# Performance work log

Hardware: AMD Instinct MI355X
Metric: run time of the kernel (lower is better)

Reference implementation:

```python
import jax, jax.numpy as jnp
import numpy as np

BITS = 8
BOUND = 2 ** (BITS - 1) - 1  # 127, symmetric int8 as in AQT IntNumerics


def setup_inputs() -> dict:
    key = jax.random.key(0)
    k1, k2 = jax.random.split(key)
    lhs = jax.random.normal(k1, (8192, 4096), dtype=jnp.float32)
    rhs = jax.random.normal(k2, (4096, 4096), dtype=jnp.float32)
    return {"lhs": lhs, "rhs": rhs}


def reference(lhs, rhs):
    # Per-channel symmetric scales over the contracting dim (AQT calibration:
    # abs-max / bound). lhs contracts axis 1, rhs contracts axis 0, per
    # dimension_numbers (((1,),(0,)),((),())).
    lhs_scale = jnp.max(jnp.abs(lhs), axis=1, keepdims=True) / BOUND  # [M,1]
    rhs_scale = jnp.max(jnp.abs(rhs), axis=0, keepdims=True) / BOUND  # [1,N]
    lhs_scale = jnp.where(lhs_scale == 0, jnp.ones_like(lhs_scale), lhs_scale)
    rhs_scale = jnp.where(rhs_scale == 0, jnp.ones_like(rhs_scale), rhs_scale)

    # Quantize: round-to-nearest, clip to [-127, 127], store as int8.
    qlhs = jnp.clip(jnp.round(lhs / lhs_scale), -BOUND, BOUND).astype(jnp.int8)
    qrhs = jnp.clip(jnp.round(rhs / rhs_scale), -BOUND, BOUND).astype(jnp.int8)

    # Integer matmul with int32 accumulation (the AQT quantized dot_general).
    acc = jax.lax.dot_general(
        qlhs, qrhs,
        dimension_numbers=(((1,), (0,)), ((), ())),
        preferred_element_type=jnp.int32,
    )  # [M, N] int32

    # Inline dequant by transposed scales (scale_t): [M,1] * [1,N].
    return acc.astype(jnp.float32) * lhs_scale * rhs_scale
```

## Files before the change

kernel.cpp:

```cpp
#include <hip/hip_runtime.h>
#include <stdint.h>

#define M_DIM 8192
#define N_DIM 4096
#define K_DIM 4096

typedef int v4i __attribute__((ext_vector_type(4)));

typedef __attribute__((address_space(1))) const void gas_void;
typedef __attribute__((address_space(3))) void las_void;

__device__ __forceinline__ void async_copy16(const uint8_t* g, uint8_t* l) {
    __builtin_amdgcn_global_load_lds((gas_void*)g, (las_void*)l, 16, 0, 0);
}

__device__ __forceinline__ int quant1(float x, float scale) {
    float q = __builtin_rintf(x / scale);
    q = fminf(127.0f, fmaxf(-127.0f, q));
    return (int)q;
}

__device__ __forceinline__ uint32_t pack4(int q0, int q1, int q2, int q3) {
    return (uint32_t)(q0 & 255) | ((uint32_t)(q1 & 255) << 8) |
           ((uint32_t)(q2 & 255) << 16) | ((uint32_t)(q3 & 255) << 24);
}

__global__ __launch_bounds__(256) void quant_lhs_kernel(
    const float* __restrict__ lhs, uint8_t* __restrict__ qlhs,
    float* __restrict__ lhs_scale) {
    const int row = blockIdx.x;
    const int tid = threadIdx.x;
    const float4* src = (const float4*)(lhs + (size_t)row * K_DIM);

    float4 v[4];
    float m = 0.0f;
#pragma unroll
    for (int i = 0; i < 4; ++i) {
        v[i] = src[tid + i * 256];
        m = fmaxf(m, fmaxf(fmaxf(fabsf(v[i].x), fabsf(v[i].y)),
                           fmaxf(fabsf(v[i].z), fabsf(v[i].w))));
    }
#pragma unroll
    for (int off = 32; off > 0; off >>= 1)
        m = fmaxf(m, __shfl_down(m, off, 64));

    __shared__ float wmax[4];
    if ((tid & 63) == 0) wmax[tid >> 6] = m;
    __syncthreads();
    const float mm = fmaxf(fmaxf(wmax[0], wmax[1]), fmaxf(wmax[2], wmax[3]));
    const float scale = (mm == 0.0f) ? 1.0f : mm / 127.0f;
    if (tid == 0) lhs_scale[row] = scale;

    uint32_t* dst = (uint32_t*)(qlhs + (size_t)row * K_DIM);
#pragma unroll
    for (int i = 0; i < 4; ++i) {
        dst[tid + i * 256] = pack4(quant1(v[i].x, scale), quant1(v[i].y, scale),
                                   quant1(v[i].z, scale), quant1(v[i].w, scale));
    }
}

__global__ __launch_bounds__(256) void rhs_max_kernel(
    const float* __restrict__ rhs, uint32_t* __restrict__ maxbits) {
    const int c = blockIdx.x * 256 + threadIdx.x;
    const int r0 = blockIdx.y * 32;
    float m = 0.0f;
#pragma unroll
    for (int r = 0; r < 32; ++r)
        m = fmaxf(m, fabsf(rhs[(size_t)(r0 + r) * N_DIM + c]));
    atomicMax(&maxbits[c], __float_as_uint(m));
}

__global__ __launch_bounds__(256) void rhs_scale_kernel(
    const uint32_t* __restrict__ maxbits, float* __restrict__ rhs_scale) {
    const int c = blockIdx.x * 256 + threadIdx.x;
    const float m = __uint_as_float(maxbits[c]);
    rhs_scale[c] = (m == 0.0f) ? 1.0f : m / 127.0f;
}

__global__ __launch_bounds__(256) void quant_rhs_t_kernel(
    const float* __restrict__ rhs, const float* __restrict__ rhs_scale,
    uint8_t* __restrict__ qrhsT) {
    __shared__ __align__(16) uint8_t tile[64 * 132];
    const int nbase = blockIdx.x * 64;
    const int kbase = blockIdx.y * 128;
    const int tid = threadIdx.x;

    const int n0 = (tid & 15) * 4;
    const float s0 = rhs_scale[nbase + n0];
    const float s1 = rhs_scale[nbase + n0 + 1];
    const float s2 = rhs_scale[nbase + n0 + 2];
    const float s3 = rhs_scale[nbase + n0 + 3];

#pragma unroll
    for (int p = 0; p < 2; ++p) {
        const int k0 = (tid >> 4) * 4 + p * 64;
        int q[4][4];
#pragma unroll
        for (int i = 0; i < 4; ++i) {
            const float4 v = *(const float4*)(
                rhs + (size_t)(kbase + k0 + i) * N_DIM + nbase + n0);
            q[i][0] = quant1(v.x, s0);
            q[i][1] = quant1(v.y, s1);
            q[i][2] = quant1(v.z, s2);
            q[i][3] = quant1(v.w, s3);
        }
#pragma unroll
        for (int j = 0; j < 4; ++j) {
            *(uint32_t*)(tile + (n0 + j) * 132 + k0) =
                pack4(q[0][j], q[1][j], q[2][j], q[3][j]);
        }
    }
    __syncthreads();

#pragma unroll
    for (int p = 0; p < 2; ++p) {
        const int c = tid + p * 256;
        const int n = c >> 3;
        const int g = c & 7;
        uint32_t d[4];
#pragma unroll
        for (int w = 0; w < 4; ++w)
            d[w] = *(const uint32_t*)(tile + n * 132 + g * 16 + w * 4);
        uint4 u;
        u.x = d[0]; u.y = d[1]; u.z = d[2]; u.w = d[3];
        *(uint4*)(qrhsT + (size_t)(nbase + n) * K_DIM + kbase + g * 16) = u;
    }
}

__global__ __launch_bounds__(256) void gemm_i8_kernel(
    const uint8_t* __restrict__ qlhs, const uint8_t* __restrict__ qrhsT,
    const float* __restrict__ lhs_scale, const float* __restrict__ rhs_scale,
    float* __restrict__ out) {
    __shared__ __align__(16) uint8_t As[128 * 64];
    __shared__ __align__(16) uint8_t Bs[128 * 64];

    const int tid = threadIdx.x;
    const int wave = tid >> 6;
    const int lane = tid & 63;

    const int bm = blockIdx.y * 128;
    const int bn = blockIdx.x * 128;

    const int srow = wave * 32 + (lane >> 2);
    const int scol = ((lane & 3) ^ ((lane >> 3) & 3)) * 16;
    const uint8_t* ga = qlhs + (size_t)(bm + srow) * K_DIM + scol;
    const uint8_t* gb = qrhsT + (size_t)(bn + srow) * K_DIM + scol;
    uint8_t* la = As + wave * 2048 + lane * 16;
    uint8_t* lb = Bs + wave * 2048 + lane * 16;
    const size_t rowstep16 = (size_t)16 * K_DIM;

    const int wm = (wave >> 1) * 64;
    const int wn = (wave & 1) * 64;
    const int fra =
        (wm + (lane & 15)) * 64 + (((lane >> 4) ^ ((lane >> 1) & 3)) * 16);
    const int frb =
        (wn + (lane & 15)) * 64 + (((lane >> 4) ^ ((lane >> 1) & 3)) * 16);

    v4i acc[4][4] = {};

    for (int k0 = 0; k0 < K_DIM; k0 += 64) {
        async_copy16(ga, la);
        async_copy16(ga + rowstep16, la + 1024);
        async_copy16(gb, lb);
        async_copy16(gb + rowstep16, lb + 1024);
        ga += 64;
        gb += 64;
        __syncthreads();

        v4i a[4], b[4];
#pragma unroll
        for (int i = 0; i < 4; ++i) a[i] = *(const v4i*)(As + fra + i * 1024);
#pragma unroll
        for (int i = 0; i < 4; ++i) b[i] = *(const v4i*)(Bs + frb + i * 1024);
#pragma unroll
        for (int mi = 0; mi < 4; ++mi)
#pragma unroll
            for (int ni = 0; ni < 4; ++ni)
                acc[mi][ni] = __builtin_amdgcn_mfma_i32_16x16x64_i8(
                    a[mi], b[ni], acc[mi][ni], 0, 0, 0);
        __syncthreads();
    }

    const int r0 = bm + wm + (lane >> 4) * 4;
    const int c0 = bn + wn + (lane & 15);
#pragma unroll
    for (int mi = 0; mi < 4; ++mi) {
        float ls[4];
#pragma unroll
        for (int r = 0; r < 4; ++r) ls[r] = lhs_scale[r0 + mi * 16 + r];
#pragma unroll
        for (int ni = 0; ni < 4; ++ni) {
            const int col = c0 + ni * 16;
            const float rs = rhs_scale[col];
            float* o = out + (size_t)(r0 + mi * 16) * N_DIM + col;
#pragma unroll
            for (int r = 0; r < 4; ++r)
                o[(size_t)r * N_DIM] = (float)acc[mi][ni][r] * ls[r] * rs;
        }
    }
}

extern "C" void kernel_launch(void* const* d_in, const int* in_sizes, int n_in,
                              void* d_out, int out_size, void* d_ws,
                              size_t ws_size, hipStream_t stream) {
    const float* lhs = (const float*)d_in[0];
    const float* rhs = (const float*)d_in[1];
    float* out = (float*)d_out;

    uint8_t* ws = (uint8_t*)d_ws;
    uint8_t* qlhs = ws;
    uint8_t* qrhsT = ws + 33554432u;
    float* lhs_scale = (float*)(ws + 50331648u);
    float* rhs_scale = (float*)(ws + 50364416u);
    uint32_t* maxbits = (uint32_t*)(ws + 50380800u);

    hipMemsetAsync(maxbits, 0, N_DIM * sizeof(uint32_t), stream);

    quant_lhs_kernel<<<M_DIM, 256, 0, stream>>>(lhs, qlhs, lhs_scale);
    rhs_max_kernel<<<dim3(N_DIM / 256, 128), 256, 0, stream>>>(rhs, maxbits);
    rhs_scale_kernel<<<N_DIM / 256, 256, 0, stream>>>(maxbits, rhs_scale);
    quant_rhs_t_kernel<<<dim3(N_DIM / 64, K_DIM / 128), 256, 0, stream>>>(
        rhs, rhs_scale, qrhsT);
    gemm_i8_kernel<<<dim3(N_DIM / 128, M_DIM / 128), 256, 0, stream>>>(
        qlhs, qrhsT, lhs_scale, rhs_scale, out);
}
```

Before: 431.6 us.

## Rewrite int8 GEMM with 256x256 tiles, 4-stage async LDS pipeline, fold rhs scale kernel

The GEMM moves to 512-thread blocks with 256x256 output tiles, 128 KB of dynamic LDS, and a four-buffer ring of global-to-LDS async copies. Loads for future K steps are issued between MFMA halves, with explicit vmcnt/lgkmcnt waits, barriers and setprio. This hides memory latency and raises arithmetic intensity compared with the old single-buffer loop that synchronised twice per step. The separate rhs_scale kernel is removed: consumers derive the scale from the max bits inline, saving a launch. The risks are higher register pressure with 32 accumulators per thread and reduced occupancy from the large LDS footprint.

```diff
diff --git a/kernel.cpp b/kernel.cpp
--- a/kernel.cpp
+++ b/kernel.cpp
@@ -70,15 +70,8 @@
     atomicMax(&maxbits[c], __float_as_uint(m));
 }
 
-__global__ __launch_bounds__(256) void rhs_scale_kernel(
-    const uint32_t* __restrict__ maxbits, float* __restrict__ rhs_scale) {
-    const int c = blockIdx.x * 256 + threadIdx.x;
-    const float m = __uint_as_float(maxbits[c]);
-    rhs_scale[c] = (m == 0.0f) ? 1.0f : m / 127.0f;
-}
-
 __global__ __launch_bounds__(256) void quant_rhs_t_kernel(
-    const float* __restrict__ rhs, const float* __restrict__ rhs_scale,
+    const float* __restrict__ rhs, const uint32_t* __restrict__ maxbits,
     uint8_t* __restrict__ qrhsT) {
     __shared__ __align__(16) uint8_t tile[64 * 132];
     const int nbase = blockIdx.x * 64;
@@ -86,10 +79,12 @@
     const int tid = threadIdx.x;
 
     const int n0 = (tid & 15) * 4;
-    const float s0 = rhs_scale[nbase + n0];
-    const float s1 = rhs_scale[nbase + n0 + 1];
-    const float s2 = rhs_scale[nbase + n0 + 2];
-    const float s3 = rhs_scale[nbase + n0 + 3];
+    float s[4];
+#pragma unroll
+    for (int j = 0; j < 4; ++j) {
+        const float m = __uint_as_float(maxbits[nbase + n0 + j]);
+        s[j] = (m == 0.0f) ? 1.0f : m / 127.0f;
+    }
 
 #pragma unroll
     for (int p = 0; p < 2; ++p) {
@@ -99,10 +94,10 @@
         for (int i = 0; i < 4; ++i) {
             const float4 v = *(const float4*)(
                 rhs + (size_t)(kbase + k0 + i) * N_DIM + nbase + n0);
-            q[i][0] = quant1(v.x, s0);
-            q[i][1] = quant1(v.y, s1);
-            q[i][2] = quant1(v.z, s2);
-            q[i][3] = quant1(v.w, s3);
+            q[i][0] = quant1(v.x, s[0]);
+            q[i][1] = quant1(v.y, s[1]);
+            q[i][2] = quant1(v.z, s[2]);
+            q[i][3] = quant1(v.w, s[3]);
         }
 #pragma unroll
         for (int j = 0; j < 4; ++j) {
@@ -127,77 +122,131 @@
     }
 }
 
-__global__ __launch_bounds__(256) void gemm_i8_kernel(
+__global__ __launch_bounds__(512, 2) void gemm_i8_kernel(
     const uint8_t* __restrict__ qlhs, const uint8_t* __restrict__ qrhsT,
-    const float* __restrict__ lhs_scale, const float* __restrict__ rhs_scale,
+    const float* __restrict__ lhs_scale, const uint32_t* __restrict__ maxbits,
     float* __restrict__ out) {
-    __shared__ __align__(16) uint8_t As[128 * 64];
-    __shared__ __align__(16) uint8_t Bs[128 * 64];
+    extern __shared__ __align__(16) uint8_t smem[];
 
     const int tid = threadIdx.x;
     const int wave = tid >> 6;
     const int lane = tid & 63;
 
-    const int bm = blockIdx.y * 128;
-    const int bn = blockIdx.x * 128;
-
-    const int srow = wave * 32 + (lane >> 2);
-    const int scol = ((lane & 3) ^ ((lane >> 3) & 3)) * 16;
-    const uint8_t* ga = qlhs + (size_t)(bm + srow) * K_DIM + scol;
-    const uint8_t* gb = qrhsT + (size_t)(bn + srow) * K_DIM + scol;
-    uint8_t* la = As + wave * 2048 + lane * 16;
-    uint8_t* lb = Bs + wave * 2048 + lane * 16;
-    const size_t rowstep16 = (size_t)16 * K_DIM;
-
-    const int wm = (wave >> 1) * 64;
-    const int wn = (wave & 1) * 64;
-    const int fra =
-        (wm + (lane & 15)) * 64 + (((lane >> 4) ^ ((lane >> 1) & 3)) * 16);
-    const int frb =
-        (wn + (lane & 15)) * 64 + (((lane >> 4) ^ ((lane >> 1) & 3)) * 16);
-
-    v4i acc[4][4] = {};
-
-    for (int k0 = 0; k0 < K_DIM; k0 += 64) {
-        async_copy16(ga, la);
-        async_copy16(ga + rowstep16, la + 1024);
-        async_copy16(gb, lb);
-        async_copy16(gb + rowstep16, lb + 1024);
-        ga += 64;
-        gb += 64;
-        __syncthreads();
-
-        v4i a[4], b[4];
-#pragma unroll
-        for (int i = 0; i < 4; ++i) a[i] = *(const v4i*)(As + fra + i * 1024);
-#pragma unroll
-        for (int i = 0; i < 4; ++i) b[i] = *(const v4i*)(Bs + frb + i * 1024);
-#pragma unroll
-        for (int mi = 0; mi < 4; ++mi)
-#pragma unroll
-            for (int ni = 0; ni < 4; ++ni)
-                acc[mi][ni] = __builtin_amdgcn_mfma_i32_16x16x64_i8(
-                    a[mi], b[ni], acc[mi][ni], 0, 0, 0);
-        __syncthreads();
-    }
+    const int bm = blockIdx.y * 256;
+    const int bn = blockIdx.x * 256;
+
+    const int srow = tid >> 2;
+    const int gsrc = (((tid & 3) ^ ((tid >> 3) & 3)) << 4);
+    const uint8_t* gA = qlhs + (size_t)(bm + srow) * K_DIM + gsrc;
+    const uint8_t* gA2 = gA + (size_t)128 * K_DIM;
+    const uint8_t* gB = qrhsT + (size_t)(bn + srow) * K_DIM + gsrc;
+    const uint8_t* gB2 = gB + (size_t)128 * K_DIM;
+    const uint32_t stO = (uint32_t)tid * 16u;
+
+    const int wm = (wave >> 2) * 128;
+    const int wn = (wave & 3) * 64;
+    const uint32_t fg = (uint32_t)((((lane >> 4) ^ ((lane >> 1) & 3)) << 4));
+    const uint32_t aoff = (uint32_t)((wm + (lane & 15)) * 64) + fg;
+    const uint32_t boff = 16384u + (uint32_t)((wn + (lane & 15)) * 64) + fg;
+
+    v4i acc[8][4] = {};
+
+#define BARRIER() __builtin_amdgcn_s_barrier()
+#define LGKM0()                                            \
+    do {                                                   \
+        asm volatile("s_waitcnt lgkmcnt(0)" ::: "memory"); \
+        __builtin_amdgcn_sched_barrier(0);                 \
+    } while (0)
+
+#pragma unroll
+    for (int p = 0; p < 3; ++p) {
+        uint8_t* sb = smem + (p << 15);
+        async_copy16(gA, sb + stO);
+        async_copy16(gA2, sb + 8192 + stO);
+        async_copy16(gB, sb + 16384 + stO);
+        async_copy16(gB2, sb + 24576 + stO);
+        gA += 64; gA2 += 64; gB += 64; gB2 += 64;
+    }
+    asm volatile("s_waitcnt vmcnt(8)" ::: "memory");
+    BARRIER();
+
+#pragma unroll 1
+    for (int tt = 0; tt < 64; tt += 4) {
+#pragma unroll
+        for (int u = 0; u < 4; ++u) {
+            const int t = tt + u;
+            uint8_t* const Cb = smem + (u << 15);
+            uint8_t* const Sb = smem + (((u + 3) & 3) << 15);
+
+            v4i a[4], b[4];
+
+#pragma unroll
+            for (int i = 0; i < 4; ++i)
+                a[i] = *(const v4i*)(Cb + aoff + i * 1024);
+#pragma unroll
+            for (int i = 0; i < 4; ++i)
+                b[i] = *(const v4i*)(Cb + boff + i * 1024);
+            async_copy16(gA, Sb + stO);
+            async_copy16(gA2, Sb + 8192 + stO);
+            BARRIER();
+            LGKM0();
+            __builtin_amdgcn_s_setprio(1);
+#pragma unroll
+            for (int mi = 0; mi < 4; ++mi)
+#pragma unroll
+                for (int ni = 0; ni < 4; ++ni)
+                    acc[mi][ni] = __builtin_amdgcn_mfma_i32_16x16x64_i8(
+                        a[mi], b[ni], acc[mi][ni], 0, 0, 0);
+            __builtin_amdgcn_s_setprio(0);
+            BARRIER();
+
+#pragma unroll
+            for (int i = 0; i < 4; ++i)
+                a[i] = *(const v4i*)(Cb + aoff + (4 + i) * 1024);
+            async_copy16(gB, Sb + 16384 + stO);
+            async_copy16(gB2, Sb + 24576 + stO);
+            if (t < 60) {
+                gA += 64; gA2 += 64; gB += 64; gB2 += 64;
+            }
+            BARRIER();
+            LGKM0();
+            __builtin_amdgcn_s_setprio(1);
+#pragma unroll
+            for (int mi = 0; mi < 4; ++mi)
+#pragma unroll
+                for (int ni = 0; ni < 4; ++ni)
+                    acc[4 + mi][ni] = __builtin_amdgcn_mfma_i32_16x16x64_i8(
+                        a[mi], b[ni], acc[4 + mi][ni], 0, 0, 0);
+            __builtin_amdgcn_s_setprio(0);
+            asm volatile("s_waitcnt vmcnt(8)" ::: "memory");
+            BARRIER();
+        }
+    }
+    asm volatile("s_waitcnt vmcnt(0)" ::: "memory");
 
     const int r0 = bm + wm + (lane >> 4) * 4;
     const int c0 = bn + wn + (lane & 15);
-#pragma unroll
-    for (int mi = 0; mi < 4; ++mi) {
+    float rsv[4];
+#pragma unroll
+    for (int ni = 0; ni < 4; ++ni) {
+        const float m = __uint_as_float(maxbits[c0 + ni * 16]);
+        rsv[ni] = (m == 0.0f) ? 1.0f : m / 127.0f;
+    }
+#pragma unroll
+    for (int mi = 0; mi < 8; ++mi) {
         float ls[4];
 #pragma unroll
         for (int r = 0; r < 4; ++r) ls[r] = lhs_scale[r0 + mi * 16 + r];
 #pragma unroll
         for (int ni = 0; ni < 4; ++ni) {
-            const int col = c0 + ni * 16;
-            const float rs = rhs_scale[col];
-            float* o = out + (size_t)(r0 + mi * 16) * N_DIM + col;
+            float* o = out + (size_t)(r0 + mi * 16) * N_DIM + c0 + ni * 16;
 #pragma unroll
             for (int r = 0; r < 4; ++r)
-                o[(size_t)r * N_DIM] = (float)acc[mi][ni][r] * ls[r] * rs;
-        }
-    }
+                o[(size_t)r * N_DIM] = (float)acc[mi][ni][r] * ls[r] * rsv[ni];
+        }
+    }
+#undef BARRIER
+#undef LGKM0
 }
 
 extern "C" void kernel_launch(void* const* d_in, const int* in_sizes, int n_in,
@@ -211,16 +260,22 @@
     uint8_t* qlhs = ws;
     uint8_t* qrhsT = ws + 33554432u;
     float* lhs_scale = (float*)(ws + 50331648u);
-    float* rhs_scale = (float*)(ws + 50364416u);
     uint32_t* maxbits = (uint32_t*)(ws + 50380800u);
+
+    static bool attr_set = false;
+    if (!attr_set) {
+        hipFuncSetAttribute((const void*)gemm_i8_kernel,
+                            hipFuncAttributeMaxDynamicSharedMemorySize,
+                            131072);
+        attr_set = true;
+    }
 
     hipMemsetAsync(maxbits, 0, N_DIM * sizeof(uint32_t), stream);
 
     quant_lhs_kernel<<<M_DIM, 256, 0, stream>>>(lhs, qlhs, lhs_scale);
     rhs_max_kernel<<<dim3(N_DIM / 256, 128), 256, 0, stream>>>(rhs, maxbits);
-    rhs_scale_kernel<<<N_DIM / 256, 256, 0, stream>>>(maxbits, rhs_scale);
     quant_rhs_t_kernel<<<dim3(N_DIM / 64, K_DIM / 128), 256, 0, stream>>>(
-        rhs, rhs_scale, qrhsT);
-    gemm_i8_kernel<<<dim3(N_DIM / 128, M_DIM / 128), 256, 0, stream>>>(
-        qlhs, qrhsT, lhs_scale, rhs_scale, out);
-}
+        rhs, maxbits, qrhsT);
+    gemm_i8_kernel<<<dim3(N_DIM / 256, M_DIM / 256), 512, 131072, stream>>>(
+        qlhs, qrhsT, lhs_scale, maxbits, out);
+}
```

New measurement: 403.7 us. -6.5%, faster.
